# Kernel optimization log

Hardware: AMD Instinct MI355X
Metric: run time of the kernel (lower is better)

Reference implementation:

```python
import jax, jax.numpy as jnp
import numpy as np

B, N, D = 4, 1024, 512
H = 8
HD = D // H  # 64
EPS = 1e-12  # F.normalize eps


def _l2_normalize(t):
    # torch.nn.functional.normalize(p=2, dim=-1): x / max(||x||_2, eps)
    nrm = jnp.sqrt(jnp.sum(t * t, axis=-1, keepdims=True))
    return t / jnp.maximum(nrm, EPS)


def setup_inputs() -> dict:
    key = jax.random.key(0)
    ks = jax.random.split(key, 5)
    scale = 1.0 / np.sqrt(D)
    inp = {
        "x": jax.random.normal(ks[0], (B, N, D), dtype=jnp.float32),
        "Wq": jax.random.normal(ks[1], (D, D), dtype=jnp.float32) * scale,
        "Wk": jax.random.normal(ks[2], (D, D), dtype=jnp.float32) * scale,
        "Wv": jax.random.normal(ks[3], (D, D), dtype=jnp.float32) * scale,
        "Wo": jax.random.normal(ks[4], (D, D), dtype=jnp.float32) * scale,
        "bq": jnp.zeros((D,), dtype=jnp.float32),
        "bk": jnp.zeros((D,), dtype=jnp.float32),
        "bv": jnp.zeros((D,), dtype=jnp.float32),
        "bo": jnp.zeros((D,), dtype=jnp.float32),
    }
    return inp


def reference(x, Wq, Wk, Wv, Wo, bq, bk, bv, bo):
    b, n, d = x.shape
    # projections (nn.Linear: x @ W.T + b), split heads -> (b, h, n, hd)
    def split_heads(t):
        return t.reshape(b, n, H, HD).transpose(0, 2, 1, 3)

    q = split_heads(x @ Wq.T + bq)
    k = split_heads(x @ Wk.T + bk)
    v = split_heads(x @ Wv.T + bv)

    q = _l2_normalize(jax.nn.elu(q))
    k = _l2_normalize(jax.nn.elu(k))

    # causal linear attention: running prefix sum of k (outer) v states
    kv_step = jnp.einsum('bhnd,bhne->bhnde', k, v)      # (b,h,n,hd,hd)
    kv_prefix = jnp.cumsum(kv_step, axis=2)             # causal prefix state
    out = jnp.einsum('bhnd,bhnde->bhne', q, kv_prefix)  # (b,h,n,hd)

    out = out.transpose(0, 2, 1, 3).reshape(b, n, d)
    return out @ Wo.T + bo
```

## Files before the change

### kernel.cpp

```cpp
#include <hip/hip_runtime.h>
#include <cmath>

#define BB 4
#define NN 1024
#define DD 512
#define HH 8
#define HDIM 64
#define ROWS (BB * NN)
#define NCHUNK 16
#define KA 512
#define WMAT ((size_t)512 * 512)

typedef _Float16 f16;
typedef f16   f16x8 __attribute__((ext_vector_type(8)));
typedef f16   f16x4 __attribute__((ext_vector_type(4)));
typedef float f32x4 __attribute__((ext_vector_type(4)));

#define GLOAD_LDS16(g, l) \
    __builtin_amdgcn_global_load_lds((const __attribute__((address_space(1))) void*)(g), \
                                     (__attribute__((address_space(3))) void*)(l), 16, 0, 0)

__global__ __launch_bounds__(256)
void split_all(const float* __restrict__ x,
               const float* __restrict__ Wq, const float* __restrict__ Wk,
               const float* __restrict__ Wv, const float* __restrict__ Wo,
               f16* __restrict__ xa, f16* __restrict__ wa)
{
    const int bid = blockIdx.x;
    const float* src;
    f16* dstbase;
    int t;
    if (bid < 2048) {
        t = bid * 256 + threadIdx.x;
        src = x;
        dstbase = xa;
    } else {
        int wb = bid - 2048;
        int m  = wb >> 8;
        t = (wb & 255) * 256 + threadIdx.x;
        src = (m == 0) ? Wq : (m == 1) ? Wk : (m == 2) ? Wv : Wo;
        dstbase = wa + (size_t)m * WMAT;
    }
    float4 v = ((const float4*)src)[t];
    int r = t >> 7;
    int c = (t & 127) * 4;
    f16x4 h;
    h[0] = (f16)v.x; h[1] = (f16)v.y; h[2] = (f16)v.z; h[3] = (f16)v.w;
    *(f16x4*)(dstbase + (size_t)r * 512 + c) = h;
}

template<int OUTMODE>
__global__ __launch_bounds__(256)
void mm_f16(const f16* __restrict__ A, const f16* __restrict__ Wm,
            const float* __restrict__ b0, const float* __restrict__ b1,
            const float* __restrict__ b2,
            f16* __restrict__ qf, f16* __restrict__ kf,
            f16* __restrict__ ktb, f16* __restrict__ vtb,
            float* __restrict__ obase)
{
    constexpr int BN = (OUTMODE == 0) ? 128 : 64;
    constexpr int NW = BN / 32;
    constexpr int BR = BN / 32;

    __shared__ __align__(16) f16 As[2][128 * 64];
    __shared__ __align__(16) f16 Bs[2][BN * 64];

    const int t    = threadIdx.x;
    const int lane = t & 63;
    const int wid  = t >> 6;
    const int wr   = wid >> 1;
    const int wc   = wid & 1;
    const int l16  = lane & 15;
    const int g16  = lane >> 4;

    const int nwg = 32 * gridDim.y;
    const int lin = blockIdx.y * 32 + blockIdx.x;
    const int swz = (lin & 7) * (nwg >> 3) + (lin >> 3);
    const int bx  = swz & 31;
    const int by  = swz >> 5;

    const int r0 = bx * 128;
    const int c0 = by * BN;
    const int z  = (OUTMODE == 0) ? (c0 >> 9) : 0;
    const int cw = (OUTMODE == 0) ? (c0 & 511) : c0;

    const f16* Wz = Wm + (size_t)z * WMAT;

    auto stage = [&](int buf, int kt) {
        const int kb = kt * 64;
        #pragma unroll
        for (int i = 0; i < 4; ++i) {
            int f = i * 256 + t;
            int row = f >> 3;
            int sc  = (f & 7) ^ (row & 7);
            GLOAD_LDS16(A + (size_t)(r0 + row) * KA + kb + sc * 8, As[buf] + f * 8);
        }
        #pragma unroll
        for (int i = 0; i < BR; ++i) {
            int f = i * 256 + t;
            int row = f >> 3;
            int sc  = (f & 7) ^ (row & 7);
            GLOAD_LDS16(Wz + (size_t)(cw + row) * KA + kb + sc * 8, Bs[buf] + f * 8);
        }
    };

    f32x4 acc[4][NW] = {};

    stage(0, 0);

    for (int kt = 0; kt < 8; ++kt) {
        const int buf = kt & 1;
        if (kt < 7) {
            stage(buf ^ 1, kt + 1);
            if (OUTMODE == 0) asm volatile("s_waitcnt vmcnt(8)" ::: "memory");
            else              asm volatile("s_waitcnt vmcnt(6)" ::: "memory");
        } else {
            asm volatile("s_waitcnt vmcnt(0)" ::: "memory");
        }
        __builtin_amdgcn_s_barrier();
        __builtin_amdgcn_sched_barrier(0);

        #pragma unroll
        for (int kk = 0; kk < 2; ++kk) {
            f16x8 af[4], bfr[NW];
            #pragma unroll
            for (int mi = 0; mi < 4; ++mi) {
                int lr = wr * 64 + mi * 16 + l16;
                int sc = (kk * 4 + g16) ^ (lr & 7);
                af[mi] = *(const f16x8*)(As[buf] + lr * 64 + sc * 8);
            }
            #pragma unroll
            for (int ni = 0; ni < NW; ++ni) {
                int lr = wc * (BN / 2) + ni * 16 + l16;
                int sc = (kk * 4 + g16) ^ (lr & 7);
                bfr[ni] = *(const f16x8*)(Bs[buf] + lr * 64 + sc * 8);
            }
            #pragma unroll
            for (int mi = 0; mi < 4; ++mi)
                #pragma unroll
                for (int ni = 0; ni < NW; ++ni)
                    acc[mi][ni] = __builtin_amdgcn_mfma_f32_16x16x32_f16(af[mi], bfr[ni], acc[mi][ni], 0, 0, 0);
        }
        __builtin_amdgcn_s_barrier();
    }

    if (OUTMODE == 1) {
        #pragma unroll
        for (int mi = 0; mi < 4; ++mi)
            #pragma unroll
            for (int ni = 0; ni < NW; ++ni) {
                int cg = c0 + wc * (BN / 2) + ni * 16 + l16;
                float bv = b0[cg];
                #pragma unroll
                for (int r = 0; r < 4; ++r) {
                    int rg = r0 + wr * 64 + mi * 16 + g16 * 4 + r;
                    obase[(size_t)rg * DD + cg] = acc[mi][ni][r] + bv;
                }
            }
    } else {
        const float* bias = (z == 0) ? b0 : (z == 1) ? b1 : b2;

        #pragma unroll
        for (int mi = 0; mi < 4; ++mi)
            #pragma unroll
            for (int ni = 0; ni < NW; ++ni) {
                float bv = bias[cw + wc * 64 + ni * 16 + l16];
                #pragma unroll
                for (int r = 0; r < 4; ++r) {
                    float v = acc[mi][ni][r] + bv;
                    if (z < 2) v = (v > 0.f) ? v : expm1f(v);
                    acc[mi][ni][r] = v;
                }
            }
        if (z < 2) {
            #pragma unroll
            for (int mi = 0; mi < 4; ++mi)
                #pragma unroll
                for (int r = 0; r < 4; ++r) {
                    float ss = 0.f;
                    #pragma unroll
                    for (int ni = 0; ni < NW; ++ni) ss += acc[mi][ni][r] * acc[mi][ni][r];
                    ss += __shfl_xor(ss, 1);
                    ss += __shfl_xor(ss, 2);
                    ss += __shfl_xor(ss, 4);
                    ss += __shfl_xor(ss, 8);
                    float sc = 1.f / fmaxf(sqrtf(ss), 1e-12f);
                    #pragma unroll
                    for (int ni = 0; ni < NW; ++ni) acc[mi][ni][r] *= sc;
                }
        }

        const int h = (cw >> 6) + wc;
        const int b = r0 >> 10;

        if (z <= 1) {
            f16* plane = (z == 0) ? qf : kf;
            #pragma unroll
            for (int mi = 0; mi < 4; ++mi)
                #pragma unroll
                for (int r = 0; r < 4; ++r) {
                    int rg = r0 + wr * 64 + mi * 16 + g16 * 4 + r;
                    f16* dst = plane + ((size_t)(b * HH + h) * NN + (rg & 1023)) * HDIM;
                    #pragma unroll
                    for (int ni = 0; ni < NW; ++ni) dst[ni * 16 + l16] = (f16)acc[mi][ni][r];
                }
        }

        if (z >= 1) {
            f16* tb = (z == 1) ? ktb : vtb;
            f16* T = (wid < 2) ? (As[0] + wid * 4096) : (Bs[0] + (wid - 2) * 4096);
            #pragma unroll
            for (int mi = 0; mi < 4; ++mi)
                #pragma unroll
                for (int ni = 0; ni < NW; ++ni)
                    #pragma unroll
                    for (int r = 0; r < 4; ++r) {
                        int n_ = mi * 16 + g16 * 4 + r;
                        int d_ = ni * 16 + l16;
                        *(f16*)((char*)T + d_ * 128 + (((n_ >> 3) ^ (d_ & 7)) * 16) + (n_ & 7) * 2)
                            = (f16)acc[mi][ni][r];
                    }
            __syncthreads();
            const int n0 = (r0 & 1023) + wr * 64;
            #pragma unroll
            for (int p = 0; p < 8; ++p) {
                int d_ = p * 8 + (lane >> 3);
                int ck = lane & 7;
                f16x8 v8 = *(const f16x8*)((char*)T + d_ * 128 + ((ck ^ (d_ & 7)) * 16));
                *(f16x8*)(tb + ((size_t)(b * HH + h) * HDIM + d_) * NN + n0 + ck * 8) = v8;
            }
        }
    }
}

__global__ __launch_bounds__(256)
void state_prefix(const f16* __restrict__ ktb, const f16* __restrict__ vtb,
                  f16* __restrict__ ptb)
{
    __shared__ __align__(16) f16 Kt[2][64 * 64];
    __shared__ __align__(16) f16 Vt[2][64 * 64];
    __shared__ __align__(16) f16 PtL[16 * 64];

    const int bh = blockIdx.x;
    const int eq = blockIdx.y;
    const int t  = threadIdx.x;
    const int lane = t & 63;
    const int wid  = t >> 6;
    const int l16  = lane & 15;
    const int g16  = lane >> 4;

    auto stage = [&](int ch, int buf) {
        #pragma unroll
        for (int i = 0; i < 2; ++i) {
            int f = i * 256 + t;
            int row = f >> 3;
            int sc  = (f & 7) ^ (row & 7);
            GLOAD_LDS16(ktb + ((size_t)bh * HDIM + row) * NN + ch * 64 + sc * 8, Kt[buf] + f * 8);
            GLOAD_LDS16(vtb + ((size_t)bh * HDIM + row) * NN + ch * 64 + sc * 8, Vt[buf] + f * 8);
        }
    };

    float pref[4] = {};
    const int d = wid * 16 + l16;

    stage(0, 0);

    for (int ch = 0; ch < NCHUNK; ++ch) {
        const int buf = ch & 1;
        stage(ch < 15 ? ch + 1 : 15, buf ^ 1);

        #pragma unroll
        for (int r = 0; r < 4; ++r) {
            int e = g16 * 4 + r;
            *(f16*)((char*)PtL + e * 128 + (((d >> 3) ^ (e & 7)) * 16) + (d & 7) * 2)
                = (f16)pref[r];
        }

        asm volatile("s_waitcnt vmcnt(4)" ::: "memory");
        asm volatile("s_waitcnt lgkmcnt(0)" ::: "memory");
        __builtin_amdgcn_s_barrier();
        __builtin_amdgcn_sched_barrier(0);

        {
            f16x4 v4 = *(const f16x4*)(PtL + t * 4);
            *(f16x4*)(ptb + (size_t)(bh * NCHUNK + ch) * 4096 + eq * 1024 + t * 4) = v4;
        }

        f32x4 sacc = {};
        #pragma unroll
        for (int ks = 0; ks < 2; ++ks) {
            int ra = eq * 16 + l16;
            f16x8 av = *(const f16x8*)(Vt[buf] + ra * 64 + ((ks * 4 + g16) ^ (ra & 7)) * 8);
            int rb = wid * 16 + l16;
            f16x8 bv = *(const f16x8*)(Kt[buf] + rb * 64 + ((ks * 4 + g16) ^ (rb & 7)) * 8);
            sacc = __builtin_amdgcn_mfma_f32_16x16x32_f16(av, bv, sacc, 0, 0, 0);
        }
        #pragma unroll
        for (int r = 0; r < 4; ++r) pref[r] += sacc[r];

        __builtin_amdgcn_s_barrier();
    }
}

__global__ __launch_bounds__(256)
void attn_chunk(const f16* __restrict__ qf, const f16* __restrict__ kf,
                const f16* __restrict__ vtb, const f16* __restrict__ ptb,
                f16* __restrict__ aug)
{
    __shared__ __align__(16) f16 Qs[64 * 64];
    __shared__ __align__(16) f16 Ks[64 * 64];
    __shared__ __align__(16) f16 Vt[64 * 64];
    __shared__ __align__(16) f16 Pt[64 * 64];
    __shared__ __align__(16) f16 Ss[64 * 64];

    const int bh = blockIdx.x;
    const int ch = blockIdx.y;
    const int t  = threadIdx.x;
    const int lane = t & 63;
    const int wid  = t >> 6;
    const int wr   = wid >> 1;
    const int wc   = wid & 1;
    const int l16  = lane & 15;
    const int g16  = lane >> 4;

    #pragma unroll
    for (int i = 0; i < 2; ++i) {
        int f = i * 256 + t;
        int row = f >> 3;
        int sc  = (f & 7) ^ (row & 7);
        GLOAD_LDS16(qf  + ((size_t)bh * NN + ch * 64 + row) * HDIM + sc * 8, Qs + f * 8);
        GLOAD_LDS16(kf  + ((size_t)bh * NN + ch * 64 + row) * HDIM + sc * 8, Ks + f * 8);
        GLOAD_LDS16(vtb + ((size_t)bh * HDIM + row) * NN + ch * 64 + sc * 8, Vt + f * 8);
        GLOAD_LDS16(ptb + (size_t)(bh * NCHUNK + ch) * 4096 + f * 8, Pt + f * 8);
    }
    __syncthreads();

    f32x4 sacc[2][2] = {};
    #pragma unroll
    for (int ks = 0; ks < 2; ++ks) {
        f16x8 af[2], bfr[2];
        #pragma unroll
        for (int mi = 0; mi < 2; ++mi) {
            int row = wr * 32 + mi * 16 + l16;
            int sc  = (ks * 4 + g16) ^ (row & 7);
            af[mi] = *(const f16x8*)(Qs + row * 64 + sc * 8);
        }
        #pragma unroll
        for (int ni = 0; ni < 2; ++ni) {
            int row = wc * 32 + ni * 16 + l16;
            int sc  = (ks * 4 + g16) ^ (row & 7);
            bfr[ni] = *(const f16x8*)(Ks + row * 64 + sc * 8);
        }
        #pragma unroll
        for (int mi = 0; mi < 2; ++mi)
            #pragma unroll
            for (int ni = 0; ni < 2; ++ni)
                sacc[mi][ni] = __builtin_amdgcn_mfma_f32_16x16x32_f16(af[mi], bfr[ni], sacc[mi][ni], 0, 0, 0);
    }
    #pragma unroll
    for (int mi = 0; mi < 2; ++mi)
        #pragma unroll
        for (int ni = 0; ni < 2; ++ni)
            #pragma unroll
            for (int r = 0; r < 4; ++r) {
                int i = wr * 32 + mi * 16 + g16 * 4 + r;
                int j = wc * 32 + ni * 16 + l16;
                float v = (j <= i) ? sacc[mi][ni][r] : 0.f;
                *(f16*)((char*)Ss + i * 128 + (((j >> 3) ^ (i & 7)) * 16) + (j & 7) * 2) = (f16)v;
            }
    __syncthreads();

    f32x4 oacc[2][2] = {};
    #pragma unroll
    for (int ks = 0; ks < 2; ++ks) {
        f16x8 af[2], bfr[2];
        #pragma unroll
        for (int mi = 0; mi < 2; ++mi) {
            int row = wr * 32 + mi * 16 + l16;
            int sc  = (ks * 4 + g16) ^ (row & 7);
            af[mi] = *(const f16x8*)(Qs + row * 64 + sc * 8);
        }
        #pragma unroll
        for (int ni = 0; ni < 2; ++ni) {
            int row = wc * 32 + ni * 16 + l16;
            int sc  = (ks * 4 + g16) ^ (row & 7);
            bfr[ni] = *(const f16x8*)(Pt + row * 64 + sc * 8);
        }
        #pragma unroll
        for (int mi = 0; mi < 2; ++mi)
            #pragma unroll
            for (int ni = 0; ni < 2; ++ni)
                oacc[mi][ni] = __builtin_amdgcn_mfma_f32_16x16x32_f16(af[mi], bfr[ni], oacc[mi][ni], 0, 0, 0);
    }
    #pragma unroll
    for (int ks = 0; ks < 2; ++ks) {
        f16x8 af[2], bfr[2];
        #pragma unroll
        for (int mi = 0; mi < 2; ++mi) {
            int row = wr * 32 + mi * 16 + l16;
            int sc  = (ks * 4 + g16) ^ (row & 7);
            af[mi] = *(const f16x8*)(Ss + row * 64 + sc * 8);
        }
        #pragma unroll
        for (int ni = 0; ni < 2; ++ni) {
            int row = wc * 32 + ni * 16 + l16;
            int sc  = (ks * 4 + g16) ^ (row & 7);
            bfr[ni] = *(const f16x8*)(Vt + row * 64 + sc * 8);
        }
        #pragma unroll
        for (int mi = 0; mi < 2; ++mi)
            #pragma unroll
            for (int ni = 0; ni < 2; ++ni)
                oacc[mi][ni] = __builtin_amdgcn_mfma_f32_16x16x32_f16(af[mi], bfr[ni], oacc[mi][ni], 0, 0, 0);
    }

    const int b = bh >> 3;
    const int h = bh & 7;
    #pragma unroll
    for (int mi = 0; mi < 2; ++mi)
        #pragma unroll
        for (int ni = 0; ni < 2; ++ni)
            #pragma unroll
            for (int r = 0; r < 4; ++r) {
                int i = wr * 32 + mi * 16 + g16 * 4 + r;
                int e = wc * 32 + ni * 16 + l16;
                aug[((size_t)(b * NN + ch * 64 + i)) * KA + h * HDIM + e] = (f16)oacc[mi][ni][r];
            }
}

extern "C" void kernel_launch(void* const* d_in, const int* in_sizes, int n_in,
                              void* d_out, int out_size, void* d_ws, size_t ws_size,
                              hipStream_t stream)
{
    (void)in_sizes; (void)n_in; (void)out_size; (void)ws_size;

    const float* x  = (const float*)d_in[0];
    const float* Wq = (const float*)d_in[1];
    const float* Wk = (const float*)d_in[2];
    const float* Wv = (const float*)d_in[3];
    const float* Wo = (const float*)d_in[4];
    const float* bq = (const float*)d_in[5];
    const float* bk = (const float*)d_in[6];
    const float* bv = (const float*)d_in[7];
    const float* bo = (const float*)d_in[8];
    float* out = (float*)d_out;

    char* ws = (char*)d_ws;
    f16* qf  = (f16*)(ws);
    f16* kf  = (f16*)(ws + (size_t)4  * 1024 * 1024);
    f16* ktb = (f16*)(ws + (size_t)8  * 1024 * 1024);
    f16* vtb = (f16*)(ws + (size_t)12 * 1024 * 1024);
    f16* ptb = (f16*)(ws + (size_t)16 * 1024 * 1024);
    f16* xa  = (f16*)(ws + (size_t)20 * 1024 * 1024);
    f16* aug = (f16*)(ws + (size_t)24 * 1024 * 1024);
    f16* wa  = (f16*)(ws + (size_t)28 * 1024 * 1024);

    dim3 blk(256);

    split_all<<<dim3(3072), blk, 0, stream>>>(x, Wq, Wk, Wv, Wo, xa, wa);

    mm_f16<0><<<dim3(32, 12), blk, 0, stream>>>(xa, wa, bq, bk, bv, qf, kf, ktb, vtb, nullptr);

    state_prefix<<<dim3(32, 4), blk, 0, stream>>>(ktb, vtb, ptb);
    attn_chunk<<<dim3(32, NCHUNK), blk, 0, stream>>>(qf, kf, vtb, ptb, aug);

    mm_f16<1><<<dim3(32, 8), blk, 0, stream>>>(aug, wa + (size_t)3 * WMAT, bo, nullptr, nullptr,
                                               nullptr, nullptr, nullptr, nullptr, out);
}
```

Baseline: 56.57 us.

## Fuse state prefix and chunk attention into one recurrent kernel

```diff
diff --git a/kernel.cpp b/kernel.cpp
--- a/kernel.cpp
+++ b/kernel.cpp
@@ -234,88 +234,21 @@
 }
 
 __global__ __launch_bounds__(256)
-void state_prefix(const f16* __restrict__ ktb, const f16* __restrict__ vtb,
-                  f16* __restrict__ ptb)
+void rec_attn(const f16* __restrict__ qf, const f16* __restrict__ kf,
+              const f16* __restrict__ ktb, const f16* __restrict__ vtb,
+              f16* __restrict__ aug)
 {
-    __shared__ __align__(16) f16 Kt[2][64 * 64];
-    __shared__ __align__(16) f16 Vt[2][64 * 64];
-    __shared__ __align__(16) f16 PtL[16 * 64];
-
-    const int bh = blockIdx.x;
-    const int eq = blockIdx.y;
-    const int t  = threadIdx.x;
-    const int lane = t & 63;
-    const int wid  = t >> 6;
-    const int l16  = lane & 15;
-    const int g16  = lane >> 4;
-
-    auto stage = [&](int ch, int buf) {
-        #pragma unroll
-        for (int i = 0; i < 2; ++i) {
-            int f = i * 256 + t;
-            int row = f >> 3;
-            int sc  = (f & 7) ^ (row & 7);
-            GLOAD_LDS16(ktb + ((size_t)bh * HDIM + row) * NN + ch * 64 + sc * 8, Kt[buf] + f * 8);
-            GLOAD_LDS16(vtb + ((size_t)bh * HDIM + row) * NN + ch * 64 + sc * 8, Vt[buf] + f * 8);
-        }
-    };
-
-    float pref[4] = {};
-    const int d = wid * 16 + l16;
-
-    stage(0, 0);
-
-    for (int ch = 0; ch < NCHUNK; ++ch) {
-        const int buf = ch & 1;
-        stage(ch < 15 ? ch + 1 : 15, buf ^ 1);
-
-        #pragma unroll
-        for (int r = 0; r < 4; ++r) {
-            int e = g16 * 4 + r;
-            *(f16*)((char*)PtL + e * 128 + (((d >> 3) ^ (e & 7)) * 16) + (d & 7) * 2)
-                = (f16)pref[r];
-        }
-
-        asm volatile("s_waitcnt vmcnt(4)" ::: "memory");
-        asm volatile("s_waitcnt lgkmcnt(0)" ::: "memory");
-        __builtin_amdgcn_s_barrier();
-        __builtin_amdgcn_sched_barrier(0);
-
-        {
-            f16x4 v4 = *(const f16x4*)(PtL + t * 4);
-            *(f16x4*)(ptb + (size_t)(bh * NCHUNK + ch) * 4096 + eq * 1024 + t * 4) = v4;
-        }
-
-        f32x4 sacc = {};
-        #pragma unroll
-        for (int ks = 0; ks < 2; ++ks) {
-            int ra = eq * 16 + l16;
-            f16x8 av = *(const f16x8*)(Vt[buf] + ra * 64 + ((ks * 4 + g16) ^ (ra & 7)) * 8);
-            int rb = wid * 16 + l16;
-            f16x8 bv = *(const f16x8*)(Kt[buf] + rb * 64 + ((ks * 4 + g16) ^ (rb & 7)) * 8);
-            sacc = __builtin_amdgcn_mfma_f32_16x16x32_f16(av, bv, sacc, 0, 0, 0);
-        }
-        #pragma unroll
-        for (int r = 0; r < 4; ++r) pref[r] += sacc[r];
-
-        __builtin_amdgcn_s_barrier();
-    }
-}
-
-__global__ __launch_bounds__(256)
-void attn_chunk(const f16* __restrict__ qf, const f16* __restrict__ kf,
-                const f16* __restrict__ vtb, const f16* __restrict__ ptb,
-                f16* __restrict__ aug)
-{
-    __shared__ __align__(16) f16 Qs[64 * 64];
-    __shared__ __align__(16) f16 Ks[64 * 64];
-    __shared__ __align__(16) f16 Vt[64 * 64];
-    __shared__ __align__(16) f16 Pt[64 * 64];
-    __shared__ __align__(16) f16 Ss[64 * 64];
-
-    const int bh = blockIdx.x;
-    const int ch = blockIdx.y;
-    const int t  = threadIdx.x;
+    __shared__ __align__(16) f16 Qs[2][4096];
+    __shared__ __align__(16) f16 Ks[2][4096];
+    __shared__ __align__(16) f16 Kt[2][4096];
+    __shared__ __align__(16) f16 Vt[2][4096];
+    __shared__ __align__(16) f16 Ss[4096];
+    __shared__ __align__(16) f16 PtL[1024];
+
+    const int bh  = blockIdx.x;
+    const int eq  = blockIdx.y;
+    const int eg0 = eq * 16;
+    const int t   = threadIdx.x;
     const int lane = t & 63;
     const int wid  = t >> 6;
     const int wr   = wid >> 1;
@@ -323,109 +256,118 @@
     const int l16  = lane & 15;
     const int g16  = lane >> 4;
 
-    #pragma unroll
-    for (int i = 0; i < 2; ++i) {
-        int f = i * 256 + t;
-        int row = f >> 3;
-        int sc  = (f & 7) ^ (row & 7);
-        GLOAD_LDS16(qf  + ((size_t)bh * NN + ch * 64 + row) * HDIM + sc * 8, Qs + f * 8);
-        GLOAD_LDS16(kf  + ((size_t)bh * NN + ch * 64 + row) * HDIM + sc * 8, Ks + f * 8);
-        GLOAD_LDS16(vtb + ((size_t)bh * HDIM + row) * NN + ch * 64 + sc * 8, Vt + f * 8);
-        GLOAD_LDS16(ptb + (size_t)(bh * NCHUNK + ch) * 4096 + f * 8, Pt + f * 8);
-    }
-    __syncthreads();
-
-    f32x4 sacc[2][2] = {};
-    #pragma unroll
-    for (int ks = 0; ks < 2; ++ks) {
-        f16x8 af[2], bfr[2];
-        #pragma unroll
-        for (int mi = 0; mi < 2; ++mi) {
-            int row = wr * 32 + mi * 16 + l16;
-            int sc  = (ks * 4 + g16) ^ (row & 7);
-            af[mi] = *(const f16x8*)(Qs + row * 64 + sc * 8);
-        }
-        #pragma unroll
-        for (int ni = 0; ni < 2; ++ni) {
-            int row = wc * 32 + ni * 16 + l16;
-            int sc  = (ks * 4 + g16) ^ (row & 7);
-            bfr[ni] = *(const f16x8*)(Ks + row * 64 + sc * 8);
-        }
-        #pragma unroll
-        for (int mi = 0; mi < 2; ++mi)
-            #pragma unroll
-            for (int ni = 0; ni < 2; ++ni)
-                sacc[mi][ni] = __builtin_amdgcn_mfma_f32_16x16x32_f16(af[mi], bfr[ni], sacc[mi][ni], 0, 0, 0);
-    }
-    #pragma unroll
-    for (int mi = 0; mi < 2; ++mi)
-        #pragma unroll
-        for (int ni = 0; ni < 2; ++ni)
-            #pragma unroll
-            for (int r = 0; r < 4; ++r) {
-                int i = wr * 32 + mi * 16 + g16 * 4 + r;
-                int j = wc * 32 + ni * 16 + l16;
-                float v = (j <= i) ? sacc[mi][ni][r] : 0.f;
-                *(f16*)((char*)Ss + i * 128 + (((j >> 3) ^ (i & 7)) * 16) + (j & 7) * 2) = (f16)v;
-            }
-    __syncthreads();
-
-    f32x4 oacc[2][2] = {};
-    #pragma unroll
-    for (int ks = 0; ks < 2; ++ks) {
-        f16x8 af[2], bfr[2];
-        #pragma unroll
-        for (int mi = 0; mi < 2; ++mi) {
-            int row = wr * 32 + mi * 16 + l16;
-            int sc  = (ks * 4 + g16) ^ (row & 7);
-            af[mi] = *(const f16x8*)(Qs + row * 64 + sc * 8);
-        }
-        #pragma unroll
-        for (int ni = 0; ni < 2; ++ni) {
-            int row = wc * 32 + ni * 16 + l16;
-            int sc  = (ks * 4 + g16) ^ (row & 7);
-            bfr[ni] = *(const f16x8*)(Pt + row * 64 + sc * 8);
-        }
-        #pragma unroll
-        for (int mi = 0; mi < 2; ++mi)
-            #pragma unroll
-            for (int ni = 0; ni < 2; ++ni)
-                oacc[mi][ni] = __builtin_amdgcn_mfma_f32_16x16x32_f16(af[mi], bfr[ni], oacc[mi][ni], 0, 0, 0);
-    }
-    #pragma unroll
-    for (int ks = 0; ks < 2; ++ks) {
-        f16x8 af[2], bfr[2];
-        #pragma unroll
-        for (int mi = 0; mi < 2; ++mi) {
-            int row = wr * 32 + mi * 16 + l16;
-            int sc  = (ks * 4 + g16) ^ (row & 7);
-            af[mi] = *(const f16x8*)(Ss + row * 64 + sc * 8);
-        }
-        #pragma unroll
-        for (int ni = 0; ni < 2; ++ni) {
-            int row = wc * 32 + ni * 16 + l16;
-            int sc  = (ks * 4 + g16) ^ (row & 7);
-            bfr[ni] = *(const f16x8*)(Vt + row * 64 + sc * 8);
-        }
-        #pragma unroll
-        for (int mi = 0; mi < 2; ++mi)
-            #pragma unroll
-            for (int ni = 0; ni < 2; ++ni)
-                oacc[mi][ni] = __builtin_amdgcn_mfma_f32_16x16x32_f16(af[mi], bfr[ni], oacc[mi][ni], 0, 0, 0);
-    }
-
+    auto stage = [&](int ch, int buf) {
+        #pragma unroll
+        for (int i = 0; i < 2; ++i) {
+            int f = i * 256 + t;
+            int row = f >> 3;
+            int sc  = (f & 7) ^ (row & 7);
+            GLOAD_LDS16(qf  + ((size_t)bh * NN + ch * 64 + row) * HDIM + sc * 8, Qs[buf] + f * 8);
+            GLOAD_LDS16(kf  + ((size_t)bh * NN + ch * 64 + row) * HDIM + sc * 8, Ks[buf] + f * 8);
+            GLOAD_LDS16(ktb + ((size_t)bh * HDIM + row) * NN + ch * 64 + sc * 8, Kt[buf] + f * 8);
+            GLOAD_LDS16(vtb + ((size_t)bh * HDIM + row) * NN + ch * 64 + sc * 8, Vt[buf] + f * 8);
+        }
+    };
+
+    float pref[4] = {};
+    const int dcol = wid * 16 + l16;
     const int b = bh >> 3;
     const int h = bh & 7;
-    #pragma unroll
-    for (int mi = 0; mi < 2; ++mi)
-        #pragma unroll
-        for (int ni = 0; ni < 2; ++ni)
-            #pragma unroll
-            for (int r = 0; r < 4; ++r) {
-                int i = wr * 32 + mi * 16 + g16 * 4 + r;
-                int e = wc * 32 + ni * 16 + l16;
-                aug[((size_t)(b * NN + ch * 64 + i)) * KA + h * HDIM + e] = (f16)oacc[mi][ni][r];
-            }
+
+    stage(0, 0);
+
+    for (int ch = 0; ch < NCHUNK; ++ch) {
+        const int buf = ch & 1;
+        if (ch < 15) stage(ch + 1, buf ^ 1);
+
+        #pragma unroll
+        for (int r = 0; r < 4; ++r) {
+            int e = g16 * 4 + r;
+            *(f16*)((char*)PtL + e * 128 + (((dcol >> 3) ^ (e & 7)) * 16) + (dcol & 7) * 2)
+                = (f16)pref[r];
+        }
+
+        if (ch == 0)      asm volatile("s_waitcnt vmcnt(8)"  ::: "memory");
+        else if (ch < 15) asm volatile("s_waitcnt vmcnt(12)" ::: "memory");
+        else              asm volatile("s_waitcnt vmcnt(0)"  ::: "memory");
+        asm volatile("s_waitcnt lgkmcnt(0)" ::: "memory");
+        __builtin_amdgcn_s_barrier();
+        __builtin_amdgcn_sched_barrier(0);
+
+        f32x4 sacc[2][2] = {};
+        #pragma unroll
+        for (int ks = 0; ks < 2; ++ks) {
+            f16x8 af[2], bfr[2];
+            #pragma unroll
+            for (int mi = 0; mi < 2; ++mi) {
+                int row = wr * 32 + mi * 16 + l16;
+                int sc  = (ks * 4 + g16) ^ (row & 7);
+                af[mi] = *(const f16x8*)(Qs[buf] + row * 64 + sc * 8);
+            }
+            #pragma unroll
+            for (int ni = 0; ni < 2; ++ni) {
+                int row = wc * 32 + ni * 16 + l16;
+                int sc  = (ks * 4 + g16) ^ (row & 7);
+                bfr[ni] = *(const f16x8*)(Ks[buf] + row * 64 + sc * 8);
+            }
+            #pragma unroll
+            for (int mi = 0; mi < 2; ++mi)
+                #pragma unroll
+                for (int ni = 0; ni < 2; ++ni)
+                    sacc[mi][ni] = __builtin_amdgcn_mfma_f32_16x16x32_f16(af[mi], bfr[ni], sacc[mi][ni], 0, 0, 0);
+        }
+        #pragma unroll
+        for (int mi = 0; mi < 2; ++mi)
+            #pragma unroll
+            for (int ni = 0; ni < 2; ++ni)
+                #pragma unroll
+                for (int r = 0; r < 4; ++r) {
+                    int i = wr * 32 + mi * 16 + g16 * 4 + r;
+                    int j = wc * 32 + ni * 16 + l16;
+                    float v = (j <= i) ? sacc[mi][ni][r] : 0.f;
+                    *(f16*)((char*)Ss + i * 128 + (((j >> 3) ^ (i & 7)) * 16) + (j & 7) * 2) = (f16)v;
+                }
+        asm volatile("s_waitcnt lgkmcnt(0)" ::: "memory");
+        __builtin_amdgcn_s_barrier();
+        __builtin_amdgcn_sched_barrier(0);
+
+        f32x4 oacc = {};
+        #pragma unroll
+        for (int ks = 0; ks < 2; ++ks) {
+            int ra = wid * 16 + l16;
+            f16x8 af = *(const f16x8*)(Qs[buf] + ra * 64 + ((ks * 4 + g16) ^ (ra & 7)) * 8);
+            f16x8 bf = *(const f16x8*)(PtL + l16 * 64 + ((ks * 4 + g16) ^ (l16 & 7)) * 8);
+            oacc = __builtin_amdgcn_mfma_f32_16x16x32_f16(af, bf, oacc, 0, 0, 0);
+        }
+        #pragma unroll
+        for (int ks = 0; ks < 2; ++ks) {
+            int ra = wid * 16 + l16;
+            int rb = eg0 + l16;
+            f16x8 af = *(const f16x8*)(Ss + ra * 64 + ((ks * 4 + g16) ^ (ra & 7)) * 8);
+            f16x8 bf = *(const f16x8*)(Vt[buf] + rb * 64 + ((ks * 4 + g16) ^ (rb & 7)) * 8);
+            oacc = __builtin_amdgcn_mfma_f32_16x16x32_f16(af, bf, oacc, 0, 0, 0);
+        }
+
+        #pragma unroll
+        for (int r = 0; r < 4; ++r) {
+            int i = wid * 16 + g16 * 4 + r;
+            aug[((size_t)(b * NN + ch * 64 + i)) * KA + h * HDIM + eg0 + l16] = (f16)oacc[r];
+        }
+
+        f32x4 up = {};
+        #pragma unroll
+        for (int ks = 0; ks < 2; ++ks) {
+            int ra = eg0 + l16;
+            int rb = wid * 16 + l16;
+            f16x8 av = *(const f16x8*)(Vt[buf] + ra * 64 + ((ks * 4 + g16) ^ (ra & 7)) * 8);
+            f16x8 bv = *(const f16x8*)(Kt[buf] + rb * 64 + ((ks * 4 + g16) ^ (rb & 7)) * 8);
+            up = __builtin_amdgcn_mfma_f32_16x16x32_f16(av, bv, up, 0, 0, 0);
+        }
+        #pragma unroll
+        for (int r = 0; r < 4; ++r) pref[r] += up[r];
+
+        __builtin_amdgcn_s_barrier();
+    }
 }
 
 extern "C" void kernel_launch(void* const* d_in, const int* in_sizes, int n_in,
@@ -450,10 +392,9 @@
     f16* kf  = (f16*)(ws + (size_t)4  * 1024 * 1024);
     f16* ktb = (f16*)(ws + (size_t)8  * 1024 * 1024);
     f16* vtb = (f16*)(ws + (size_t)12 * 1024 * 1024);
-    f16* ptb = (f16*)(ws + (size_t)16 * 1024 * 1024);
-    f16* xa  = (f16*)(ws + (size_t)20 * 1024 * 1024);
-    f16* aug = (f16*)(ws + (size_t)24 * 1024 * 1024);
-    f16* wa  = (f16*)(ws + (size_t)28 * 1024 * 1024);
+    f16* xa  = (f16*)(ws + (size_t)16 * 1024 * 1024);
+    f16* aug = (f16*)(ws + (size_t)20 * 1024 * 1024);
+    f16* wa  = (f16*)(ws + (size_t)24 * 1024 * 1024);
 
     dim3 blk(256);
 
@@ -461,8 +402,7 @@
 
     mm_f16<0><<<dim3(32, 12), blk, 0, stream>>>(xa, wa, bq, bk, bv, qf, kf, ktb, vtb, nullptr);
 
-    state_prefix<<<dim3(32, 4), blk, 0, stream>>>(ktb, vtb, ptb);
-    attn_chunk<<<dim3(32, NCHUNK), blk, 0, stream>>>(qf, kf, vtb, ptb, aug);
+    rec_attn<<<dim3(32, 4), blk, 0, stream>>>(qf, kf, ktb, vtb, aug);
 
     mm_f16<1><<<dim3(32, 8), blk, 0, stream>>>(aug, wa + (size_t)3 * WMAT, bo, nullptr, nullptr,
                                                nullptr, nullptr, nullptr, nullptr, out);
```

After: 62.67 us. +10.8%, slower.
